# Kernel tuning notes

Measured on AMD Instinct MI355X. Metric: run time of the kernel, lower is better.

The kernel has to match this reference:

```python
import jax, jax.numpy as jnp
import numpy as np


def setup_inputs() -> dict:
    key = jax.random.key(0)
    k1, k2 = jax.random.split(key)
    embedding = jax.random.normal(k1, (8192, 256), dtype=jnp.float32)
    label = jax.random.randint(k2, (8192,), 0, 1000, dtype=jnp.int64 if jax.config.jax_enable_x64 else jnp.int32)
    return {"embedding": embedding, "label": label}


def reference(embedding, label):
    # embedding: [B, W]; label is unused by the original module's math.
    B, W = embedding.shape
    miu = embedding.mean(axis=0)                      # [W]
    ec = embedding - miu                              # [B, W] centered
    # mean over batch of outer products ec[b] ec[b]^T == (ec^T @ ec) / B
    cov = jnp.einsum('bi,bj->ij', ec, ec) / B         # [W, W]
    diff = cov - jnp.eye(W, dtype=embedding.dtype)
    loss = jnp.sqrt(jnp.sum(diff * diff))             # Frobenius norm
    return loss
```

## Files before the change

### kernel.cpp

```cpp
#include <hip/hip_runtime.h>
#include <math.h>

#define BROWS 8192
#define WDIM 256
#define NTILES 10
#define CHUNKS 64
#define CHUNK_ROWS 128
#define NSTAGES 8
#define TILE_ELEMS 4096
#define FIN_BLOCKS 160

static __device__ const int g_tile_ti[NTILES] = {0,0,0,0,1,1,1,2,2,3};
static __device__ const int g_tile_tj[NTILES] = {0,1,2,3,1,2,3,2,3,3};


__global__ __launch_bounds__(256)
void gram_kernel(const float* __restrict__ E, float* __restrict__ ws) {
    float* colsum   = ws;
    float* partials = ws + 512;

    const int t = blockIdx.x;
    const int c = blockIdx.y;
    const int ti = g_tile_ti[t], tj = g_tile_tj[t];
    const int tid = threadIdx.x;
    const int tx = tid & 15, ty = tid >> 4;

    __shared__ __align__(16) float a_s[16][64];
    __shared__ __align__(16) float b_s[16][64];

    const int row0 = c * CHUNK_ROWS;
    const float* Ea = E + ti * 64;
    const float* Eb = E + tj * 64;

    float acc[4][4];
    #pragma unroll
    for (int ii = 0; ii < 4; ++ii)
        #pragma unroll
        for (int jj = 0; jj < 4; ++jj) acc[ii][jj] = 0.f;
    float4 cs = make_float4(0.f, 0.f, 0.f, 0.f);

    float4 pa, pb;
    {
        const size_t r = (size_t)(row0 + ty);
        pa = *(const float4*)(Ea + r * WDIM + tx * 4);
        pb = *(const float4*)(Eb + r * WDIM + tx * 4);
    }

    for (int s = 0; s < NSTAGES; ++s) {
        __syncthreads();
        *(float4*)&a_s[ty][tx * 4] = pa;
        *(float4*)&b_s[ty][tx * 4] = pb;
        cs.x += pa.x; cs.y += pa.y; cs.z += pa.z; cs.w += pa.w;
        if (s + 1 < NSTAGES) {
            const size_t r = (size_t)(row0 + (s + 1) * 16 + ty);
            pa = *(const float4*)(Ea + r * WDIM + tx * 4);
            pb = *(const float4*)(Eb + r * WDIM + tx * 4);
        }
        __syncthreads();
        #pragma unroll
        for (int k = 0; k < 16; ++k) {
            const float4 a4 = *(const float4*)&a_s[k][ty * 4];
            const float4 b4 = *(const float4*)&b_s[k][tx * 4];
            const float av[4] = {a4.x, a4.y, a4.z, a4.w};
            const float bv[4] = {b4.x, b4.y, b4.z, b4.w};
            #pragma unroll
            for (int ii = 0; ii < 4; ++ii)
                #pragma unroll
                for (int jj = 0; jj < 4; ++jj)
                    acc[ii][jj] = fmaf(av[ii], bv[jj], acc[ii][jj]);
        }
    }

    float* dst = partials + (size_t)(c * NTILES + t) * TILE_ELEMS;
    #pragma unroll
    for (int ii = 0; ii < 4; ++ii) {
        const float4 v = make_float4(acc[ii][0], acc[ii][1], acc[ii][2], acc[ii][3]);
        *(float4*)(dst + (ty * 4 + ii) * 64 + tx * 4) = v;
    }

    if (ti == tj) {
        __syncthreads();
        *(float4*)&a_s[ty][tx * 4] = cs;
        __syncthreads();
        if (tid < 64) {
            float s = 0.f;
            #pragma unroll
            for (int r = 0; r < 16; ++r) s += a_s[r][tid];
            atomicAdd(&colsum[ti * 64 + tid], s);
        }
    }
}

__global__ __launch_bounds__(256)
void finalize_kernel(float* __restrict__ ws, float* __restrict__ out) {
    const float* colsum   = ws;
    float* lossacc        = ws + 256;
    unsigned* done        = (unsigned*)(ws + 257);
    const float* partials = ws + 512;

    const int e = blockIdx.x * 256 + threadIdx.x;
    const int t = e >> 12;
    const int local = e & 4095;
    const int ti = g_tile_ti[t], tj = g_tile_tj[t];
    const int i = ti * 64 + (local >> 6);
    const int j = tj * 64 + (local & 63);

    float g = 0.f;
    #pragma unroll 8
    for (int c = 0; c < CHUNKS; ++c)
        g += partials[(size_t)(c * NTILES + t) * TILE_ELEMS + local];

    const float inv_b = 1.0f / (float)BROWS;
    const float mi = colsum[i] * inv_b;
    const float mj = colsum[j] * inv_b;
    const float diff = g * inv_b - mi * mj - ((i == j) ? 1.0f : 0.0f);
    float v = ((ti == tj) ? 1.0f : 2.0f) * diff * diff;

    #pragma unroll
    for (int o = 32; o > 0; o >>= 1) v += __shfl_down(v, o, 64);

    __shared__ float red[4];
    if ((threadIdx.x & 63) == 0) red[threadIdx.x >> 6] = v;
    __syncthreads();
    if (threadIdx.x == 0) {
        const float s = red[0] + red[1] + red[2] + red[3];
        atomicAdd(lossacc, s);
        __threadfence();
        const unsigned old = atomicAdd(done, 1u);
        if (old == FIN_BLOCKS - 1) {
            const float total = atomicAdd(lossacc, 0.0f);
            out[0] = sqrtf(total);
        }
    }
}

extern "C" void kernel_launch(void* const* d_in, const int* in_sizes, int n_in,
                              void* d_out, int out_size, void* d_ws, size_t ws_size,
                              hipStream_t stream) {
    const float* E = (const float*)d_in[0];
    float* out = (float*)d_out;
    float* ws = (float*)d_ws;

    hipMemsetAsync(d_ws, 0, 512 * sizeof(float), stream);
    gram_kernel<<<dim3(NTILES, CHUNKS), 256, 0, stream>>>(E, ws);
    finalize_kernel<<<FIN_BLOCKS, 256, 0, stream>>>(ws, out);
}
```

Before: 82.36 us.

## Use 128x128 gram tiles with 8x8 register blocking over short row chunks

Replaces the ten 64x64 upper-triangular tiles with three 128x128 tiles. Each thread now computes an 8x8 sub-block, and diagonal tiles reuse A as B to skip a load. Row chunks shrink to 32 rows staged in one shot, which removes the staged pipeline and its per-stage syncs. In exchange the partial-sum buffer grows several-fold, so the finalize pass must read many more partials.

After: 92.00 us. 11.7% more time.

```diff
diff --git a/kernel.cpp b/kernel.cpp
--- a/kernel.cpp
+++ b/kernel.cpp
@@ -3,15 +3,11 @@
 
 #define BROWS 8192
 #define WDIM 256
-#define NTILES 10
-#define CHUNKS 64
-#define CHUNK_ROWS 128
-#define NSTAGES 8
-#define TILE_ELEMS 4096
-#define FIN_BLOCKS 160
-
-static __device__ const int g_tile_ti[NTILES] = {0,0,0,0,1,1,1,2,2,3};
-static __device__ const int g_tile_tj[NTILES] = {0,1,2,3,1,2,3,2,3,3};
+#define NT 3
+#define CHUNKS 256
+#define CHUNK_ROWS 32
+#define TILE_ELEMS 16384
+#define FIN_BLOCKS 192
 
 
 __global__ __launch_bounds__(256)
@@ -21,74 +17,101 @@
 
     const int t = blockIdx.x;
     const int c = blockIdx.y;
-    const int ti = g_tile_ti[t], tj = g_tile_tj[t];
+    const int ti = (t == 2) ? 1 : 0;
+    const int tj = (t == 0) ? 0 : 1;
+    const bool diag = (t != 1);
     const int tid = threadIdx.x;
     const int tx = tid & 15, ty = tid >> 4;
 
-    __shared__ __align__(16) float a_s[16][64];
-    __shared__ __align__(16) float b_s[16][64];
+    __shared__ __align__(16) float lds[9216];
+    float* As = lds;
+    float* Bs = lds + 4096;
+    float* Cs = lds + 8192;
 
     const int row0 = c * CHUNK_ROWS;
-    const float* Ea = E + ti * 64;
-    const float* Eb = E + tj * 64;
+    const float* Ea = E + ti * 128;
+    const float* Eb = E + tj * 128;
 
-    float acc[4][4];
+    float4 ga[4], gb[4];
     #pragma unroll
-    for (int ii = 0; ii < 4; ++ii)
+    for (int s = 0; s < 2; ++s)
         #pragma unroll
-        for (int jj = 0; jj < 4; ++jj) acc[ii][jj] = 0.f;
-    float4 cs = make_float4(0.f, 0.f, 0.f, 0.f);
+        for (int i = 0; i < 2; ++i) {
+            const int p = tid + i * 256;
+            const int r = p >> 5, c4 = p & 31;
+            const size_t gr = (size_t)(row0 + s * 16 + r) * WDIM;
+            ga[s * 2 + i] = *(const float4*)(Ea + gr + c4 * 4);
+            if (!diag) gb[s * 2 + i] = *(const float4*)(Eb + gr + c4 * 4);
+        }
 
-    float4 pa, pb;
-    {
-        const size_t r = (size_t)(row0 + ty);
-        pa = *(const float4*)(Ea + r * WDIM + tx * 4);
-        pb = *(const float4*)(Eb + r * WDIM + tx * 4);
+    #pragma unroll
+    for (int s = 0; s < 2; ++s)
+        #pragma unroll
+        for (int i = 0; i < 2; ++i) {
+            const int p = tid + i * 256;
+            const int r = p >> 5, c4 = p & 31;
+            *(float4*)&As[s * 2048 + r * 128 + c4 * 4] = ga[s * 2 + i];
+            if (!diag) *(float4*)&Bs[s * 2048 + r * 128 + c4 * 4] = gb[s * 2 + i];
+        }
+    if (diag) {
+        float4 cs;
+        cs.x = ga[0].x + ga[1].x + ga[2].x + ga[3].x;
+        cs.y = ga[0].y + ga[1].y + ga[2].y + ga[3].y;
+        cs.z = ga[0].z + ga[1].z + ga[2].z + ga[3].z;
+        cs.w = ga[0].w + ga[1].w + ga[2].w + ga[3].w;
+        *(float4*)&Cs[(tid >> 5) * 128 + (tid & 31) * 4] = cs;
     }
 
-    for (int s = 0; s < NSTAGES; ++s) {
-        __syncthreads();
-        *(float4*)&a_s[ty][tx * 4] = pa;
-        *(float4*)&b_s[ty][tx * 4] = pb;
-        cs.x += pa.x; cs.y += pa.y; cs.z += pa.z; cs.w += pa.w;
-        if (s + 1 < NSTAGES) {
-            const size_t r = (size_t)(row0 + (s + 1) * 16 + ty);
-            pa = *(const float4*)(Ea + r * WDIM + tx * 4);
-            pb = *(const float4*)(Eb + r * WDIM + tx * 4);
-        }
-        __syncthreads();
+    __syncthreads();
+
+    if (diag && tid < 128) {
+        float s = 0.f;
         #pragma unroll
+        for (int m = 0; m < 8; ++m) s += Cs[m * 128 + tid];
+        atomicAdd(&colsum[ti * 128 + tid], s);
+    }
+
+    const float* Bp = diag ? As : Bs;
+    float acc[8][8];
+    #pragma unroll
+    for (int ii = 0; ii < 8; ++ii)
+        #pragma unroll
+        for (int jj = 0; jj < 8; ++jj) acc[ii][jj] = 0.f;
+
+    #pragma unroll
+    for (int s2 = 0; s2 < 2; ++s2) {
+        const int sb = s2 * 2048;
+        #pragma unroll 4
         for (int k = 0; k < 16; ++k) {
-            const float4 a4 = *(const float4*)&a_s[k][ty * 4];
-            const float4 b4 = *(const float4*)&b_s[k][tx * 4];
-            const float av[4] = {a4.x, a4.y, a4.z, a4.w};
-            const float bv[4] = {b4.x, b4.y, b4.z, b4.w};
+            const float4 a0 = *(const float4*)&As[sb + k * 128 + ty * 4];
+            const float4 a1 = *(const float4*)&As[sb + k * 128 + 64 + ty * 4];
+            const float4 b0 = *(const float4*)&Bp[sb + k * 128 + tx * 4];
+            const float4 b1 = *(const float4*)&Bp[sb + k * 128 + 64 + tx * 4];
+            const float av[8] = {a0.x, a0.y, a0.z, a0.w, a1.x, a1.y, a1.z, a1.w};
+            const float bv[8] = {b0.x, b0.y, b0.z, b0.w, b1.x, b1.y, b1.z, b1.w};
             #pragma unroll
-            for (int ii = 0; ii < 4; ++ii)
+            for (int ii = 0; ii < 8; ++ii)
                 #pragma unroll
-                for (int jj = 0; jj < 4; ++jj)
+                for (int jj = 0; jj < 8; ++jj)
                     acc[ii][jj] = fmaf(av[ii], bv[jj], acc[ii][jj]);
         }
     }
 
-    float* dst = partials + (size_t)(c * NTILES + t) * TILE_ELEMS;
+    float* dst = partials + (size_t)(c * NT + t) * TILE_ELEMS;
     #pragma unroll
-    for (int ii = 0; ii < 4; ++ii) {
-        const float4 v = make_float4(acc[ii][0], acc[ii][1], acc[ii][2], acc[ii][3]);
-        *(float4*)(dst + (ty * 4 + ii) * 64 + tx * 4) = v;
-    }
-
-    if (ti == tj) {
-        __syncthreads();
-        *(float4*)&a_s[ty][tx * 4] = cs;
-        __syncthreads();
-        if (tid < 64) {
-            float s = 0.f;
+    for (int ri = 0; ri < 2; ++ri)
+        #pragma unroll
+        for (int ii = 0; ii < 4; ++ii)
             #pragma unroll
-            for (int r = 0; r < 16; ++r) s += a_s[r][tid];
-            atomicAdd(&colsum[ti * 64 + tid], s);
-        }
-    }
+            for (int ci = 0; ci < 2; ++ci) {
+                const int row = ri * 64 + ty * 4 + ii;
+                const int colg = ci * 64 + tx * 4;
+                const float4 v = make_float4(acc[ri * 4 + ii][ci * 4 + 0],
+                                             acc[ri * 4 + ii][ci * 4 + 1],
+                                             acc[ri * 4 + ii][ci * 4 + 2],
+                                             acc[ri * 4 + ii][ci * 4 + 3]);
+                *(float4*)(dst + row * 128 + colg) = v;
+            }
 }
 
 __global__ __launch_bounds__(256)
@@ -99,22 +122,23 @@
     const float* partials = ws + 512;
 
     const int e = blockIdx.x * 256 + threadIdx.x;
-    const int t = e >> 12;
-    const int local = e & 4095;
-    const int ti = g_tile_ti[t], tj = g_tile_tj[t];
-    const int i = ti * 64 + (local >> 6);
-    const int j = tj * 64 + (local & 63);
+    const int t = e >> 14;
+    const int local = e & 16383;
+    const int ti = (t == 2) ? 1 : 0;
+    const int tj = (t == 0) ? 0 : 1;
+    const int i = ti * 128 + (local >> 7);
+    const int j = tj * 128 + (local & 127);
 
     float g = 0.f;
-    #pragma unroll 8
+    #pragma unroll 32
     for (int c = 0; c < CHUNKS; ++c)
-        g += partials[(size_t)(c * NTILES + t) * TILE_ELEMS + local];
+        g += partials[(size_t)(c * NT + t) * TILE_ELEMS + local];
 
     const float inv_b = 1.0f / (float)BROWS;
     const float mi = colsum[i] * inv_b;
     const float mj = colsum[j] * inv_b;
     const float diff = g * inv_b - mi * mj - ((i == j) ? 1.0f : 0.0f);
-    float v = ((ti == tj) ? 1.0f : 2.0f) * diff * diff;
+    float v = ((t == 1) ? 2.0f : 1.0f) * diff * diff;
 
     #pragma unroll
     for (int o = 32; o > 0; o >>= 1) v += __shfl_down(v, o, 64);
@@ -128,6 +152,7 @@
         __threadfence();
         const unsigned old = atomicAdd(done, 1u);
         if (old == FIN_BLOCKS - 1) {
+            __threadfence();
             const float total = atomicAdd(lossacc, 0.0f);
             out[0] = sqrtf(total);
         }
@@ -142,6 +167,6 @@
     float* ws = (float*)d_ws;
 
     hipMemsetAsync(d_ws, 0, 512 * sizeof(float), stream);
-    gram_kernel<<<dim3(NTILES, CHUNKS), 256, 0, stream>>>(E, ws);
+    gram_kernel<<<dim3(NT, CHUNKS), 256, 0, stream>>>(E, ws);
     finalize_kernel<<<FIN_BLOCKS, 256, 0, stream>>>(ws, out);
 }
```

## Use bf16 MFMA Gram with transposed cast pre-pass and larger tiles

Applied to the files above, without the earlier changes.

Adds a pre-pass that casts the embedding to bf16, writes a transposed copy, and computes per-row-group column sums in place of atomics. The Gram kernel then uses 32x32x16 bf16 MFMA instructions over three 128x128 upper-triangle tiles, in place of scalar FP32 FMAs over ten 64x64 tiles. The memset is dropped and the finalize kernel reduces the column sums itself. The aim is to move the matmul onto matrix cores, at the cost of bf16 rounding error in the covariance and an extra kernel launch with a round trip through global memory.

After: 83.43 us. Within noise of the previous version (+1.3%).

```diff
diff --git a/kernel.cpp b/kernel.cpp
--- a/kernel.cpp
+++ b/kernel.cpp
@@ -1,135 +1,171 @@
 #include <hip/hip_runtime.h>
 #include <math.h>
 
+typedef unsigned int uint32;
+typedef unsigned short ushort16;
+typedef __bf16 bf16x8 __attribute__((ext_vector_type(8)));
+typedef float f32x16 __attribute__((ext_vector_type(16)));
+
 #define BROWS 8192
 #define WDIM 256
-#define NTILES 10
+#define NT 3
 #define CHUNKS 64
-#define CHUNK_ROWS 128
-#define NSTAGES 8
-#define TILE_ELEMS 4096
-#define FIN_BLOCKS 160
+#define CHUNK_K 128
+#define TILE_ELEMS 16384
+#define FIN_BLOCKS 192
 
-static __device__ const int g_tile_ti[NTILES] = {0,0,0,0,1,1,1,2,2,3};
-static __device__ const int g_tile_tj[NTILES] = {0,1,2,3,1,2,3,2,3,3};
+#define WS_LOSS 8192
+#define WS_DONE 8193
+#define WS_PART 8448
+#define WS_ET   3154176
 
+__device__ __forceinline__ uint32 pack2bf(float lo, float hi) {
+    uint32 a = __float_as_uint(lo), b = __float_as_uint(hi);
+    a = (a + 0x7FFFu + ((a >> 16) & 1u)) >> 16;
+    b = (b + 0x7FFFu + ((b >> 16) & 1u)) >> 16;
+    return a | (b << 16);
+}
 
 __global__ __launch_bounds__(256)
-void gram_kernel(const float* __restrict__ E, float* __restrict__ ws) {
-    float* colsum   = ws;
-    float* partials = ws + 512;
+void cast_t_kernel(const float* __restrict__ E, float* __restrict__ ws) {
+    const int cg = blockIdx.x;
+    const int rg = blockIdx.y;
+    const int tid = threadIdx.x;
+    __shared__ uint32 U[64 * 129];
+    __shared__ float Cs[16 * 64];
 
-    const int t = blockIdx.x;
-    const int c = blockIdx.y;
-    const int ti = g_tile_ti[t], tj = g_tile_tj[t];
-    const int tid = threadIdx.x;
-    const int tx = tid & 15, ty = tid >> 4;
+    if (cg == 0 && rg == 0 && tid < 2) ws[WS_LOSS + tid] = 0.0f;
 
-    __shared__ __align__(16) float a_s[16][64];
-    __shared__ __align__(16) float b_s[16][64];
+    const int c4 = tid & 15;
+    const int rp = tid >> 4;
+    const float* Eb = E + (size_t)(rg * 256) * WDIM + cg * 64;
 
-    const int row0 = c * CHUNK_ROWS;
-    const float* Ea = E + ti * 64;
-    const float* Eb = E + tj * 64;
+    float4 cs = make_float4(0.f, 0.f, 0.f, 0.f);
+    #pragma unroll
+    for (int p = 0; p < 8; ++p) {
+        const int rpi = rp + 16 * p;
+        const int r0 = 2 * rpi;
+        const float4 fa = *(const float4*)(Eb + (size_t)r0 * WDIM + c4 * 4);
+        const float4 fb = *(const float4*)(Eb + (size_t)(r0 + 1) * WDIM + c4 * 4);
+        cs.x += fa.x + fb.x; cs.y += fa.y + fb.y;
+        cs.z += fa.z + fb.z; cs.w += fa.w + fb.w;
+        U[(c4 * 4 + 0) * 129 + rpi] = pack2bf(fa.x, fb.x);
+        U[(c4 * 4 + 1) * 129 + rpi] = pack2bf(fa.y, fb.y);
+        U[(c4 * 4 + 2) * 129 + rpi] = pack2bf(fa.z, fb.z);
+        U[(c4 * 4 + 3) * 129 + rpi] = pack2bf(fa.w, fb.w);
+    }
+    *(float4*)&Cs[rp * 64 + c4 * 4] = cs;
+    __syncthreads();
 
-    float acc[4][4];
-    #pragma unroll
-    for (int ii = 0; ii < 4; ++ii)
+    if (tid < 64) {
+        float s = 0.f;
         #pragma unroll
-        for (int jj = 0; jj < 4; ++jj) acc[ii][jj] = 0.f;
-    float4 cs = make_float4(0.f, 0.f, 0.f, 0.f);
-
-    float4 pa, pb;
-    {
-        const size_t r = (size_t)(row0 + ty);
-        pa = *(const float4*)(Ea + r * WDIM + tx * 4);
-        pb = *(const float4*)(Eb + r * WDIM + tx * 4);
+        for (int r = 0; r < 16; ++r) s += Cs[r * 64 + tid];
+        ws[rg * WDIM + cg * 64 + tid] = s;
     }
 
-    for (int s = 0; s < NSTAGES; ++s) {
-        __syncthreads();
-        *(float4*)&a_s[ty][tx * 4] = pa;
-        *(float4*)&b_s[ty][tx * 4] = pb;
-        cs.x += pa.x; cs.y += pa.y; cs.z += pa.z; cs.w += pa.w;
-        if (s + 1 < NSTAGES) {
-            const size_t r = (size_t)(row0 + (s + 1) * 16 + ty);
-            pa = *(const float4*)(Ea + r * WDIM + tx * 4);
-            pb = *(const float4*)(Eb + r * WDIM + tx * 4);
-        }
-        __syncthreads();
-        #pragma unroll
-        for (int k = 0; k < 16; ++k) {
-            const float4 a4 = *(const float4*)&a_s[k][ty * 4];
-            const float4 b4 = *(const float4*)&b_s[k][tx * 4];
-            const float av[4] = {a4.x, a4.y, a4.z, a4.w};
-            const float bv[4] = {b4.x, b4.y, b4.z, b4.w};
-            #pragma unroll
-            for (int ii = 0; ii < 4; ++ii)
-                #pragma unroll
-                for (int jj = 0; jj < 4; ++jj)
-                    acc[ii][jj] = fmaf(av[ii], bv[jj], acc[ii][jj]);
-        }
-    }
-
-    float* dst = partials + (size_t)(c * NTILES + t) * TILE_ELEMS;
+    uint32* Et = (uint32*)(ws + WS_ET);
+    const int col = tid >> 2, sub = tid & 3;
+    uint32* dstc = Et + (size_t)(cg * 64 + col) * 4096 + rg * 128 + sub * 32;
+    const uint32* Uc = U + col * 129 + sub * 32;
     #pragma unroll
-    for (int ii = 0; ii < 4; ++ii) {
-        const float4 v = make_float4(acc[ii][0], acc[ii][1], acc[ii][2], acc[ii][3]);
-        *(float4*)(dst + (ty * 4 + ii) * 64 + tx * 4) = v;
-    }
-
-    if (ti == tj) {
-        __syncthreads();
-        *(float4*)&a_s[ty][tx * 4] = cs;
-        __syncthreads();
-        if (tid < 64) {
-            float s = 0.f;
-            #pragma unroll
-            for (int r = 0; r < 16; ++r) s += a_s[r][tid];
-            atomicAdd(&colsum[ti * 64 + tid], s);
-        }
+    for (int j = 0; j < 8; ++j) {
+        uint4 v;
+        v.x = Uc[4 * j + 0]; v.y = Uc[4 * j + 1];
+        v.z = Uc[4 * j + 2]; v.w = Uc[4 * j + 3];
+        *(uint4*)(dstc + 4 * j) = v;
     }
 }
 
 __global__ __launch_bounds__(256)
+void gram_kernel(float* __restrict__ ws) {
+    const ushort16* Et = (const ushort16*)(ws + WS_ET);
+    float* partials = ws + WS_PART;
+    const int t = blockIdx.x, c = blockIdx.y;
+    const int ti = (t == 2) ? 1 : 0;
+    const int tj = (t == 0) ? 0 : 1;
+    const int tid = threadIdx.x, w = tid >> 6, l = tid & 63;
+    const int lm = l & 31;
+    const int lk = (l >> 5) * 8;
+    const size_t CS = 8192;
+
+    const ushort16* ap = Et + (size_t)(ti * 128 + w * 32 + lm) * CS + (size_t)c * CHUNK_K + lk;
+    const ushort16* bp = Et + (size_t)(tj * 128 + lm) * CS + (size_t)c * CHUNK_K + lk;
+
+    f32x16 acc[4];
+    #pragma unroll
+    for (int n = 0; n < 4; ++n)
+        #pragma unroll
+        for (int r = 0; r < 16; ++r) acc[n][r] = 0.f;
+
+    #pragma unroll
+    for (int s = 0; s < 8; ++s) {
+        const int o = s * 16;
+        const bf16x8 a  = *(const bf16x8*)(ap + o);
+        const bf16x8 b0 = *(const bf16x8*)(bp + o);
+        const bf16x8 b1 = *(const bf16x8*)(bp + 32 * CS + o);
+        const bf16x8 b2 = *(const bf16x8*)(bp + 64 * CS + o);
+        const bf16x8 b3 = *(const bf16x8*)(bp + 96 * CS + o);
+        acc[0] = __builtin_amdgcn_mfma_f32_32x32x16_bf16(a, b0, acc[0], 0, 0, 0);
+        acc[1] = __builtin_amdgcn_mfma_f32_32x32x16_bf16(a, b1, acc[1], 0, 0, 0);
+        acc[2] = __builtin_amdgcn_mfma_f32_32x32x16_bf16(a, b2, acc[2], 0, 0, 0);
+        acc[3] = __builtin_amdgcn_mfma_f32_32x32x16_bf16(a, b3, acc[3], 0, 0, 0);
+    }
+
+    float* dst = partials + ((size_t)c * NT + t) * TILE_ELEMS;
+    const int rbase = 32 * w + 4 * (l >> 5);
+    #pragma unroll
+    for (int n = 0; n < 4; ++n)
+        #pragma unroll
+        for (int r = 0; r < 16; ++r) {
+            const int row = rbase + (r & 3) + 8 * (r >> 2);
+            dst[row * 128 + n * 32 + lm] = acc[n][r];
+        }
+}
+
+__global__ __launch_bounds__(256)
 void finalize_kernel(float* __restrict__ ws, float* __restrict__ out) {
-    const float* colsum   = ws;
-    float* lossacc        = ws + 256;
-    unsigned* done        = (unsigned*)(ws + 257);
-    const float* partials = ws + 512;
+    __shared__ float mu[WDIM];
+    __shared__ float red[4];
+    const float* partials = ws + WS_PART;
+    float* lossacc = ws + WS_LOSS;
+    unsigned* done = (unsigned*)(ws + WS_DONE);
+    const int tid = threadIdx.x;
 
-    const int e = blockIdx.x * 256 + threadIdx.x;
-    const int t = e >> 12;
-    const int local = e & 4095;
-    const int ti = g_tile_ti[t], tj = g_tile_tj[t];
-    const int i = ti * 64 + (local >> 6);
-    const int j = tj * 64 + (local & 63);
+    {
+        float s = 0.f;
+        #pragma unroll 8
+        for (int rg = 0; rg < 32; ++rg) s += ws[rg * WDIM + tid];
+        mu[tid] = s * (1.0f / (float)BROWS);
+    }
+    __syncthreads();
+
+    const int e = blockIdx.x * 256 + tid;
+    const int t = e >> 14, local = e & 16383;
+    const int ti = (t == 2) ? 1 : 0;
+    const int tj = (t == 0) ? 0 : 1;
+    const int i = ti * 128 + (local >> 7);
+    const int j = tj * 128 + (local & 127);
 
     float g = 0.f;
     #pragma unroll 8
     for (int c = 0; c < CHUNKS; ++c)
-        g += partials[(size_t)(c * NTILES + t) * TILE_ELEMS + local];
+        g += partials[((size_t)c * NT + t) * TILE_ELEMS + local];
 
-    const float inv_b = 1.0f / (float)BROWS;
-    const float mi = colsum[i] * inv_b;
-    const float mj = colsum[j] * inv_b;
-    const float diff = g * inv_b - mi * mj - ((i == j) ? 1.0f : 0.0f);
-    float v = ((ti == tj) ? 1.0f : 2.0f) * diff * diff;
+    const float diff = g * (1.0f / (float)BROWS) - mu[i] * mu[j] - ((i == j) ? 1.0f : 0.0f);
+    float v = ((t == 1) ? 2.0f : 1.0f) * diff * diff;
 
     #pragma unroll
     for (int o = 32; o > 0; o >>= 1) v += __shfl_down(v, o, 64);
-
-    __shared__ float red[4];
-    if ((threadIdx.x & 63) == 0) red[threadIdx.x >> 6] = v;
+    if ((tid & 63) == 0) red[tid >> 6] = v;
     __syncthreads();
-    if (threadIdx.x == 0) {
-        const float s = red[0] + red[1] + red[2] + red[3];
-        atomicAdd(lossacc, s);
+    if (tid == 0) {
+        atomicAdd(lossacc, red[0] + red[1] + red[2] + red[3]);
         __threadfence();
         const unsigned old = atomicAdd(done, 1u);
         if (old == FIN_BLOCKS - 1) {
-            const float total = atomicAdd(lossacc, 0.0f);
-            out[0] = sqrtf(total);
+            __threadfence();
+            out[0] = sqrtf(atomicAdd(lossacc, 0.0f));
         }
     }
 }
@@ -141,7 +177,7 @@
     float* out = (float*)d_out;
     float* ws = (float*)d_ws;
 
-    hipMemsetAsync(d_ws, 0, 512 * sizeof(float), stream);
-    gram_kernel<<<dim3(NTILES, CHUNKS), 256, 0, stream>>>(E, ws);
+    cast_t_kernel<<<dim3(4, 32), 256, 0, stream>>>(E, ws);
+    gram_kernel<<<dim3(NT, CHUNKS), 256, 0, stream>>>(ws);
     finalize_kernel<<<FIN_BLOCKS, 256, 0, stream>>>(ws, out);
 }
```
